# Optimization experiments

Hardware: AMD Instinct MI355X
Metric: run time of the kernel (lower is better)

The kernel has to match this reference:

```python
import jax, jax.numpy as jnp
import numpy as np

DIM = 1024
HEADS = 16
DIM_HEAD = 64
INNER = HEADS * DIM_HEAD
SCALE = DIM_HEAD ** -0.5


def setup_inputs() -> dict:
    key = jax.random.key(0)
    kx, kq, kk, kv, ko = jax.random.split(key, 5)
    B, N = 2, 2048
    s = DIM ** -0.5
    return {
        "x": jax.random.normal(kx, (B, N, DIM), dtype=jnp.float32),
        "Wq": jax.random.normal(kq, (DIM, INNER), dtype=jnp.float32) * s,
        "Wk": jax.random.normal(kk, (DIM, INNER), dtype=jnp.float32) * s,
        "Wv": jax.random.normal(kv, (DIM, INNER), dtype=jnp.float32) * s,
        "Wo": jax.random.normal(ko, (INNER, DIM), dtype=jnp.float32) * s,
    }


def reference(x, Wq, Wk, Wv, Wo):
    B, N, _ = x.shape
    # projections, split heads: b n (h d) -> b h n d
    def split(t):
        return t.reshape(B, N, HEADS, DIM_HEAD).transpose(0, 2, 1, 3)
    q = split(x @ Wq)
    k = split(x @ Wk)
    v = split(x @ Wv)
    # scores [B,H,N,N]
    dots = jnp.einsum("bhnd,bhmd->bhnm", q, k) * SCALE
    # causal mask: positions j > i masked
    causal = jnp.triu(jnp.ones((N, N), dtype=bool), k=1)
    dots = jnp.where(causal, -jnp.inf, dots)
    attn = jax.nn.softmax(dots, axis=-1)
    out = jnp.einsum("bhnm,bhmd->bhnd", attn, v)
    out = out.transpose(0, 2, 1, 3).reshape(B, N, INNER)
    return out @ Wo
```

## Files before the change

kernel.cpp:

```cpp
#include <hip/hip_runtime.h>

typedef unsigned short u16;
typedef unsigned int u32;
typedef __attribute__((ext_vector_type(8))) short short8;
typedef __attribute__((ext_vector_type(4))) short s16x4;
typedef __attribute__((ext_vector_type(4))) float f32x4;
typedef __attribute__((ext_vector_type(16))) float f32x16;
typedef __attribute__((ext_vector_type(4))) u32 u32x4;

typedef const __attribute__((address_space(1))) void* gptr_t;
typedef __attribute__((address_space(3))) void* sptr_t;

#define N_SEQ 2048
#define DIM 1024
#define INNER 1024
#define NTOK 4096
#define QKV_LD 3072

__device__ __forceinline__ u16 f2b(float f) {
  union { float f; unsigned u; } v; v.f = f;
  unsigned r = v.u + 0x7fffu + ((v.u >> 16) & 1u);
  return (u16)(r >> 16);
}

__global__ __launch_bounds__(256) void cast_x_kernel(const float* __restrict__ src,
                                                     u16* __restrict__ dst) {
  const size_t i = (size_t)blockIdx.x * 256 + threadIdx.x;
  const f32x4* s = (const f32x4*)(src + i * 8);
  f32x4 a = s[0], b = s[1];
  short8 o;
#pragma unroll
  for (int j = 0; j < 4; ++j) { o[j] = (short)f2b(a[j]); o[4 + j] = (short)f2b(b[j]); }
  *(short8*)(dst + i * 8) = o;
}

__global__ __launch_bounds__(256) void transpose_cast_kernel(const float* __restrict__ src,
                                                             u16* __restrict__ dst) {
  __shared__ u16 tile[64][65];
  const int n0 = blockIdx.x * 64, k0 = blockIdx.y * 64;
  for (int i = threadIdx.x; i < 4096; i += 256) {
    const int r = i >> 6, c = i & 63;
    tile[r][c] = f2b(src[(size_t)(k0 + r) * 1024 + n0 + c]);
  }
  __syncthreads();
  for (int i = threadIdx.x; i < 4096; i += 256) {
    const int r = i >> 6, c = i & 63;
    dst[(size_t)(n0 + r) * 1024 + k0 + c] = tile[c][r];
  }
}

__global__ __launch_bounds__(256) void transpose_v_kernel(const u16* __restrict__ qkv,
                                                          u16* __restrict__ vt) {
  __shared__ u16 t[64][72];
  const int nt0 = blockIdx.x * 64;
  const int bh = blockIdx.y;
  const int b = bh >> 4, h = bh & 15;
  const u16* src = qkv + (size_t)b * N_SEQ * QKV_LD + 2048 + h * 64;
#pragma unroll
  for (int i = 0; i < 2; ++i) {
    const int cid = i * 256 + threadIdx.x;
    const int r = cid >> 3, c = (cid & 7) * 8;
    *(short8*)&t[r][c] = *(const short8*)(src + (size_t)(nt0 + r) * QKV_LD + c);
  }
  __syncthreads();
#pragma unroll
  for (int i = 0; i < 2; ++i) {
    const int cid = i * 256 + threadIdx.x;
    const int d = cid >> 3, c = (cid & 7) * 8;
    short8 v;
#pragma unroll
    for (int j = 0; j < 8; ++j) v[j] = t[c + j][d];
    *(short8*)(vt + ((size_t)bh * 64 + d) * N_SEQ + nt0 + c) = v;
  }
}

template <typename OutT>
__global__ __launch_bounds__(256) void gemm_tn(const u16* __restrict__ A,
                                               const u16* __restrict__ Bt,
                                               OutT* __restrict__ C,
                                               int M, int N, int K) {
  __shared__ u16 Al[128 * 64];
  __shared__ u16 Bl[128 * 64];
  const int tid = threadIdx.x;
  const int w = tid >> 6, lane = tid & 63;
  const int l15 = lane & 15, lg = lane >> 4;
  const int wr = w >> 1, wc = w & 1;
  const int nwg = gridDim.x * gridDim.y;
  int bid = blockIdx.y * gridDim.x + blockIdx.x;
  bid = (bid & 7) * (nwg >> 3) + (bid >> 3);
  const int bx = bid % gridDim.x, by = bid / gridDim.x;
  const int m0 = by * 128, n0 = bx * 128;

  f32x4 acc[4][4] = {};

  for (int k0 = 0; k0 < K; k0 += 64) {
#pragma unroll
    for (int i = 0; i < 4; ++i) {
      const int chunk = (w << 2) + i;
      const int e = (chunk << 9) + lane * 8;
      const int row = e >> 6, col = e & 63;
      const u16* ga = A + (size_t)(m0 + row) * K + k0 + col;
      __builtin_amdgcn_global_load_lds((gptr_t)ga, (sptr_t)(Al + (chunk << 9)), 16, 0, 0);
      const u16* gb = Bt + (size_t)(n0 + row) * K + k0 + col;
      __builtin_amdgcn_global_load_lds((gptr_t)gb, (sptr_t)(Bl + (chunk << 9)), 16, 0, 0);
    }
    __syncthreads();
#pragma unroll
    for (int kk = 0; kk < 2; ++kk) {
      short8 af[4], bf[4];
#pragma unroll
      for (int m = 0; m < 4; ++m)
        af[m] = *(const short8*)(Al + ((wr * 64 + m * 16 + l15) << 6) + kk * 32 + lg * 8);
#pragma unroll
      for (int n = 0; n < 4; ++n)
        bf[n] = *(const short8*)(Bl + ((wc * 64 + n * 16 + l15) << 6) + kk * 32 + lg * 8);
#pragma unroll
      for (int m = 0; m < 4; ++m)
#pragma unroll
        for (int n = 0; n < 4; ++n)
          acc[m][n] = __builtin_amdgcn_mfma_f32_16x16x32_bf16(af[m], bf[n], acc[m][n], 0, 0, 0);
    }
    __syncthreads();
  }

#pragma unroll
  for (int m = 0; m < 4; ++m)
#pragma unroll
    for (int n = 0; n < 4; ++n)
#pragma unroll
      for (int r = 0; r < 4; ++r) {
        const int row = m0 + wr * 64 + m * 16 + lg * 4 + r;
        const int col = n0 + wc * 64 + n * 16 + l15;
        const float v = acc[m][n][r];
        if constexpr (sizeof(OutT) == 2) C[(size_t)row * N + col] = (OutT)f2b(v);
        else                             C[(size_t)row * N + col] = (OutT)v;
      }
}

__global__ __launch_bounds__(256) void attn_kernel(const u16* __restrict__ qkv,
                                                   const u16* __restrict__ vt,
                                                   u16* __restrict__ attnb) {
  const int bh = blockIdx.x;
  const int qt = 15 - (int)blockIdx.y;
  const int b = bh >> 4, h = bh & 15;
  const int tid = threadIdx.x;
  const int lane = tid & 63, w = tid >> 6;
  const int l31 = lane & 31, hh = lane >> 5;
  const int q0 = qt * 128;
  const int qrow = q0 + w * 32 + l31;

  __shared__ u16 Kl[128 * 64];
  __shared__ u16 Vl[64 * 128];

  const u16* base  = qkv + (size_t)b * N_SEQ * QKV_LD;
  const u16* kbase = base + 1024 + h * 64;
  const u16* vbase = vt + (size_t)bh * 64 * N_SEQ;

  short8 bq[4];
#pragma unroll
  for (int ks = 0; ks < 4; ++ks)
    bq[ks] = *(const short8*)(base + (size_t)qrow * QKV_LD + h * 64 + ks * 16 + hh * 8);

  f32x16 o0 = {}, o1 = {};
  float m_run = -3.0e38f, l_run = 0.f;
  const float kscale = 0.125f * 1.4426950408889634f;
  const int nt = qt + 1;
  const int wbase = tid & ~63;

  for (int jt = 0; jt < nt; ++jt) {
    const int kv0 = jt * 128;
    __syncthreads();
#pragma unroll
    for (int i = 0; i < 4; ++i) {
      const int cid = i * 256 + tid;
      const int krow = cid >> 3, kc = (cid & 7) ^ (krow & 7);
      const u16* ks = kbase + (size_t)(kv0 + krow) * QKV_LD + kc * 8;
      __builtin_amdgcn_global_load_lds((gptr_t)ks, (sptr_t)(Kl + (i * 256 + wbase) * 8), 16, 0, 0);
      const int vrow = cid >> 4, vc = (cid & 15) ^ (vrow & 15);
      const u16* vs = vbase + (size_t)vrow * N_SEQ + kv0 + vc * 8;
      __builtin_amdgcn_global_load_lds((gptr_t)vs, (sptr_t)(Vl + (i * 256 + wbase) * 8), 16, 0, 0);
    }
    __syncthreads();

    const bool last = (jt == nt - 1);
#pragma unroll
    for (int sub = 0; sub < 2; ++sub) {
      if (last && sub == 1 && w < 2) continue;
      const int kv0s = kv0 + sub * 64;

      f32x16 p0 = {}, p1 = {};
#pragma unroll
      for (int ks = 0; ks < 4; ++ks) {
        const int r0 = sub * 64 + l31;
        const int r1 = r0 + 32;
        short8 ak0 = *(const short8*)(Kl + r0 * 64 + (((ks * 2 + hh) ^ (r0 & 7)) * 8));
        short8 ak1 = *(const short8*)(Kl + r1 * 64 + (((ks * 2 + hh) ^ (r1 & 7)) * 8));
        p0 = __builtin_amdgcn_mfma_f32_32x32x16_bf16(ak0, bq[ks], p0, 0, 0, 0);
        p1 = __builtin_amdgcn_mfma_f32_32x32x16_bf16(ak1, bq[ks], p1, 0, 0, 0);
      }

      if (last) {
        const int kvb = kv0s + 4 * hh;
#pragma unroll
        for (int r = 0; r < 16; ++r) {
          const int off = (r & 3) + 8 * (r >> 2);
          if (kvb + off > qrow)      p0[r] = -3.0e38f;
          if (kvb + 32 + off > qrow) p1[r] = -3.0e38f;
        }
      }

      float mt = -3.0e38f;
#pragma unroll
      for (int r = 0; r < 16; ++r) { mt = fmaxf(mt, p0[r]); mt = fmaxf(mt, p1[r]); }
      mt = fmaxf(mt, __shfl_xor(mt, 32, 64));
      const float mn = fmaxf(m_run, mt);
      const float sf = exp2f((m_run - mn) * kscale);
      m_run = mn;
      float ps = 0.f;
#pragma unroll
      for (int r = 0; r < 16; ++r) {
        const float e0 = exp2f((p0[r] - mn) * kscale);
        const float e1 = exp2f((p1[r] - mn) * kscale);
        p0[r] = e0; p1[r] = e1;
        ps += e0 + e1;
      }
      ps += __shfl_xor(ps, 32, 64);
      l_run = l_run * sf + ps;
      o0 *= sf; o1 *= sf;

      u32 bpw[4][4];
#define PACK_TILE(P, kf)                                                    \
      {                                                                     \
        _Pragma("unroll")                                                   \
        for (int a2 = 0; a2 < 2; ++a2) {                                    \
          _Pragma("unroll")                                                 \
          for (int c2 = 0; c2 < 2; ++c2) {                                  \
            u32 X, Y;                                                       \
            asm("v_cvt_pk_bf16_f32 %0, %1, %2" : "=v"(X)                    \
                : "v"(P[8 * a2 + 2 * c2]), "v"(P[8 * a2 + 2 * c2 + 1]));    \
            asm("v_cvt_pk_bf16_f32 %0, %1, %2" : "=v"(Y)                    \
                : "v"(P[8 * a2 + 4 + 2 * c2]), "v"(P[8 * a2 + 5 + 2 * c2]));\
            asm("v_permlane32_swap_b32 %0, %1" : "+v"(X), "+v"(Y));         \
            bpw[(kf) * 2 + a2][c2] = X;                   \
            bpw[(kf) * 2 + a2][2 + c2] = Y;               \
          }                                                                 \
        }                                                                   \
      }
      PACK_TILE(p0, 0)
      PACK_TILE(p1, 1)
#undef PACK_TILE

#pragma unroll
      for (int ks16 = 0; ks16 < 4; ++ks16) {
        u32x4 t = {bpw[ks16][0], bpw[ks16][1], bpw[ks16][2], bpw[ks16][3]};
        short8 bp = __builtin_bit_cast(short8, t);
        const int cb = sub * 8 + ks16 * 2 + hh;
        const int row0 = l31;
        const int row1 = 32 + l31;
        short8 av0 = *(const short8*)(Vl + row0 * 128 + ((cb ^ (row0 & 15)) * 8));
        short8 av1 = *(const short8*)(Vl + row1 * 128 + ((cb ^ (row1 & 15)) * 8));
        o0 = __builtin_amdgcn_mfma_f32_32x32x16_bf16(av0, bp, o0, 0, 0, 0);
        o1 = __builtin_amdgcn_mfma_f32_32x32x16_bf16(av1, bp, o1, 0, 0, 0);
      }
    }
  }

  const float inv = 1.f / l_run;
  u16* orow = attnb + ((size_t)b * N_SEQ + qrow) * INNER + h * 64 + 4 * hh;
#pragma unroll
  for (int rq = 0; rq < 4; ++rq) {
    s16x4 sv0, sv1;
#pragma unroll
    for (int j = 0; j < 4; ++j) {
      sv0[j] = (short)f2b(o0[rq * 4 + j] * inv);
      sv1[j] = (short)f2b(o1[rq * 4 + j] * inv);
    }
    *(s16x4*)(orow + rq * 8) = sv0;
    *(s16x4*)(orow + 32 + rq * 8) = sv1;
  }
}

extern "C" void kernel_launch(void* const* d_in, const int* in_sizes, int n_in,
                              void* d_out, int out_size, void* d_ws, size_t ws_size,
                              hipStream_t stream) {
  const float* x  = (const float*)d_in[0];
  const float* Wq = (const float*)d_in[1];
  const float* Wk = (const float*)d_in[2];
  const float* Wv = (const float*)d_in[3];
  const float* Wo = (const float*)d_in[4];
  float* out = (float*)d_out;

  u16* xb    = (u16*)d_ws;
  u16* wqkvt = xb    + (size_t)NTOK * DIM;
  u16* wot   = wqkvt + (size_t)3 * INNER * DIM;
  u16* qkv   = wot   + (size_t)DIM * INNER;
  u16* attnb = qkv   + (size_t)NTOK * QKV_LD;
  u16* vtb   = attnb + (size_t)NTOK * INNER;

  cast_x_kernel<<<dim3(NTOK * DIM / (256 * 8)), 256, 0, stream>>>(x, xb);
  transpose_cast_kernel<<<dim3(16, 16), 256, 0, stream>>>(Wq, wqkvt);
  transpose_cast_kernel<<<dim3(16, 16), 256, 0, stream>>>(Wk, wqkvt + (size_t)1024 * 1024);
  transpose_cast_kernel<<<dim3(16, 16), 256, 0, stream>>>(Wv, wqkvt + (size_t)2048 * 1024);
  transpose_cast_kernel<<<dim3(16, 16), 256, 0, stream>>>(Wo, wot);

  gemm_tn<u16><<<dim3(3072 / 128, 4096 / 128), 256, 0, stream>>>(xb, wqkvt, qkv, NTOK, 3072, DIM);
  transpose_v_kernel<<<dim3(32, 32), 256, 0, stream>>>(qkv, vtb);
  attn_kernel<<<dim3(32, 16), 256, 0, stream>>>(qkv, vtb, attnb);
  gemm_tn<float><<<dim3(1024 / 128, 4096 / 128), 256, 0, stream>>>(attnb, wot, out, NTOK, INNER, INNER);
}
```

Before: 158.8 us.

## Double-buffer K/V tiles in attention, add lazy softmax rescale and MFMA priority

Switches the attention kernel's K/V shared-memory tiles to double buffering. The next tile is prefetched with global_load_lds while the current tile is computed, so each iteration no longer waits on its load between two barriers. It also skips the running-max rescale of the output accumulators unless the max grows past a threshold, and raises wave priority around the MFMA loops. The cost is doubled LDS use, which may lower occupancy, and hand-written vmcnt waits whose correctness depends on exact load counts.

```diff
diff --git a/kernel.cpp b/kernel.cpp
--- a/kernel.cpp
+++ b/kernel.cpp
@@ -149,8 +149,8 @@
   const int q0 = qt * 128;
   const int qrow = q0 + w * 32 + l31;
 
-  __shared__ u16 Kl[128 * 64];
-  __shared__ u16 Vl[64 * 128];
+  __shared__ u16 Kl[2][128 * 64];
+  __shared__ u16 Vl[2][64 * 128];
 
   const u16* base  = qkv + (size_t)b * N_SEQ * QKV_LD;
   const u16* kbase = base + 1024 + h * 64;
@@ -167,21 +167,40 @@
   const int nt = qt + 1;
   const int wbase = tid & ~63;
 
+#define STAGE(jt_, bufsel)                                                          \
+  {                                                                                 \
+    const int kv0_ = (jt_) * 128;                                                   \
+    u16* Klb = Kl[bufsel];                                                          \
+    u16* Vlb = Vl[bufsel];                                                          \
+    _Pragma("unroll")                                                               \
+    for (int i = 0; i < 4; ++i) {                                                   \
+      const int cid = i * 256 + tid;                                                \
+      const int krow = cid >> 3, kc = (cid & 7) ^ (krow & 7);                       \
+      const u16* ksp = kbase + (size_t)(kv0_ + krow) * QKV_LD + kc * 8;             \
+      __builtin_amdgcn_global_load_lds((gptr_t)ksp,                                 \
+          (sptr_t)(Klb + (i * 256 + wbase) * 8), 16, 0, 0);                         \
+      const int vrow = cid >> 4, vc = (cid & 15) ^ (vrow & 15);                     \
+      const u16* vsp = vbase + (size_t)vrow * N_SEQ + kv0_ + vc * 8;                \
+      __builtin_amdgcn_global_load_lds((gptr_t)vsp,                                 \
+          (sptr_t)(Vlb + (i * 256 + wbase) * 8), 16, 0, 0);                         \
+    }                                                                               \
+  }
+
+  STAGE(0, 0)
+
   for (int jt = 0; jt < nt; ++jt) {
     const int kv0 = jt * 128;
-    __syncthreads();
-#pragma unroll
-    for (int i = 0; i < 4; ++i) {
-      const int cid = i * 256 + tid;
-      const int krow = cid >> 3, kc = (cid & 7) ^ (krow & 7);
-      const u16* ks = kbase + (size_t)(kv0 + krow) * QKV_LD + kc * 8;
-      __builtin_amdgcn_global_load_lds((gptr_t)ks, (sptr_t)(Kl + (i * 256 + wbase) * 8), 16, 0, 0);
-      const int vrow = cid >> 4, vc = (cid & 15) ^ (vrow & 15);
-      const u16* vs = vbase + (size_t)vrow * N_SEQ + kv0 + vc * 8;
-      __builtin_amdgcn_global_load_lds((gptr_t)vs, (sptr_t)(Vl + (i * 256 + wbase) * 8), 16, 0, 0);
-    }
-    __syncthreads();
-
+    const int cur = jt & 1;
+    if (jt + 1 < nt) {
+      STAGE(jt + 1, cur ^ 1)
+      asm volatile("s_waitcnt vmcnt(8)" ::: "memory");
+    } else {
+      asm volatile("s_waitcnt vmcnt(0)" ::: "memory");
+    }
+    __builtin_amdgcn_s_barrier();
+
+    const u16* Klb = Kl[cur];
+    const u16* Vlb = Vl[cur];
     const bool last = (jt == nt - 1);
 #pragma unroll
     for (int sub = 0; sub < 2; ++sub) {
@@ -189,15 +208,17 @@
       const int kv0s = kv0 + sub * 64;
 
       f32x16 p0 = {}, p1 = {};
+      __builtin_amdgcn_s_setprio(1);
 #pragma unroll
       for (int ks = 0; ks < 4; ++ks) {
         const int r0 = sub * 64 + l31;
         const int r1 = r0 + 32;
-        short8 ak0 = *(const short8*)(Kl + r0 * 64 + (((ks * 2 + hh) ^ (r0 & 7)) * 8));
-        short8 ak1 = *(const short8*)(Kl + r1 * 64 + (((ks * 2 + hh) ^ (r1 & 7)) * 8));
+        short8 ak0 = *(const short8*)(Klb + r0 * 64 + (((ks * 2 + hh) ^ (r0 & 7)) * 8));
+        short8 ak1 = *(const short8*)(Klb + r1 * 64 + (((ks * 2 + hh) ^ (r1 & 7)) * 8));
         p0 = __builtin_amdgcn_mfma_f32_32x32x16_bf16(ak0, bq[ks], p0, 0, 0, 0);
         p1 = __builtin_amdgcn_mfma_f32_32x32x16_bf16(ak1, bq[ks], p1, 0, 0, 0);
       }
+      __builtin_amdgcn_s_setprio(0);
 
       if (last) {
         const int kvb = kv0s + 4 * hh;
@@ -214,19 +235,22 @@
       for (int r = 0; r < 16; ++r) { mt = fmaxf(mt, p0[r]); mt = fmaxf(mt, p1[r]); }
       mt = fmaxf(mt, __shfl_xor(mt, 32, 64));
       const float mn = fmaxf(m_run, mt);
-      const float sf = exp2f((m_run - mn) * kscale);
-      m_run = mn;
+      if (!__all(mn - m_run <= 44.f)) {
+        const float sf = exp2f((m_run - mn) * kscale);
+        m_run = mn;
+        l_run *= sf;
+        o0 *= sf; o1 *= sf;
+      }
       float ps = 0.f;
 #pragma unroll
       for (int r = 0; r < 16; ++r) {
-        const float e0 = exp2f((p0[r] - mn) * kscale);
-        const float e1 = exp2f((p1[r] - mn) * kscale);
+        const float e0 = exp2f((p0[r] - m_run) * kscale);
+        const float e1 = exp2f((p1[r] - m_run) * kscale);
         p0[r] = e0; p1[r] = e1;
         ps += e0 + e1;
       }
       ps += __shfl_xor(ps, 32, 64);
-      l_run = l_run * sf + ps;
-      o0 *= sf; o1 *= sf;
+      l_run += ps;
 
       u32 bpw[4][4];
 #define PACK_TILE(P, kf)                                                    \
@@ -241,8 +265,8 @@
             asm("v_cvt_pk_bf16_f32 %0, %1, %2" : "=v"(Y)                    \
                 : "v"(P[8 * a2 + 4 + 2 * c2]), "v"(P[8 * a2 + 5 + 2 * c2]));\
             asm("v_permlane32_swap_b32 %0, %1" : "+v"(X), "+v"(Y));         \
-            bpw[(kf) * 2 + a2][c2] = X;                   \
-            bpw[(kf) * 2 + a2][2 + c2] = Y;               \
+            bpw[(kf) * 2 + a2][c2] = X;                                     \
+            bpw[(kf) * 2 + a2][2 + c2] = Y;                                 \
           }                                                                 \
         }                                                                   \
       }
@@ -250,6 +274,7 @@
       PACK_TILE(p1, 1)
 #undef PACK_TILE
 
+      __builtin_amdgcn_s_setprio(1);
 #pragma unroll
       for (int ks16 = 0; ks16 < 4; ++ks16) {
         u32x4 t = {bpw[ks16][0], bpw[ks16][1], bpw[ks16][2], bpw[ks16][3]};
@@ -257,13 +282,16 @@
         const int cb = sub * 8 + ks16 * 2 + hh;
         const int row0 = l31;
         const int row1 = 32 + l31;
-        short8 av0 = *(const short8*)(Vl + row0 * 128 + ((cb ^ (row0 & 15)) * 8));
-        short8 av1 = *(const short8*)(Vl + row1 * 128 + ((cb ^ (row1 & 15)) * 8));
+        short8 av0 = *(const short8*)(Vlb + row0 * 128 + ((cb ^ (row0 & 15)) * 8));
+        short8 av1 = *(const short8*)(Vlb + row1 * 128 + ((cb ^ (row1 & 15)) * 8));
         o0 = __builtin_amdgcn_mfma_f32_32x32x16_bf16(av0, bp, o0, 0, 0, 0);
         o1 = __builtin_amdgcn_mfma_f32_32x32x16_bf16(av1, bp, o1, 0, 0, 0);
       }
-    }
-  }
+      __builtin_amdgcn_s_setprio(0);
+    }
+    __builtin_amdgcn_s_barrier();
+  }
+#undef STAGE
 
   const float inv = 1.f / l_run;
   u16* orow = attnb + ((size_t)b * N_SEQ + qrow) * INNER + h * 64 + 4 * hh;
```

After: 164.0 us. 1.03x slower.

## Drop LDS staging in attention; per-wave direct K/V loads with lazy rescale

Applied to the files above, without the earlier changes.

Removes the shared-memory K/V tiles and block-wide barriers so each wave independently loads its 64-key K and V fragments straight from global memory into registers. Each wave now runs over only its own causal range, using 64-key steps. It also adds lazy softmax rescaling, which skips the exp and accumulator rescale unless the max rises past a threshold, and adds s_setprio around the MFMA bursts. The trade is that waves in a block no longer share K/V loads, so global/L2 traffic rises and latency may be exposed without a software pipeline.

```diff
diff --git a/kernel.cpp b/kernel.cpp
--- a/kernel.cpp
+++ b/kernel.cpp
@@ -141,16 +141,13 @@
                                                    const u16* __restrict__ vt,
                                                    u16* __restrict__ attnb) {
   const int bh = blockIdx.x;
-  const int qt = 15 - (int)blockIdx.y;
   const int b = bh >> 4, h = bh & 15;
   const int tid = threadIdx.x;
   const int lane = tid & 63, w = tid >> 6;
   const int l31 = lane & 31, hh = lane >> 5;
-  const int q0 = qt * 128;
-  const int qrow = q0 + w * 32 + l31;
-
-  __shared__ u16 Kl[128 * 64];
-  __shared__ u16 Vl[64 * 128];
+  const int qw = (15 - (int)blockIdx.y) * 4 + w;
+  const int q0 = qw * 32;
+  const int qrow = q0 + l31;
 
   const u16* base  = qkv + (size_t)b * N_SEQ * QKV_LD;
   const u16* kbase = base + 1024 + h * 64;
@@ -164,105 +161,100 @@
   f32x16 o0 = {}, o1 = {};
   float m_run = -3.0e38f, l_run = 0.f;
   const float kscale = 0.125f * 1.4426950408889634f;
-  const int nt = qt + 1;
-  const int wbase = tid & ~63;
+  const int nt = (qw >> 1) + 1;
 
   for (int jt = 0; jt < nt; ++jt) {
-    const int kv0 = jt * 128;
-    __syncthreads();
-#pragma unroll
-    for (int i = 0; i < 4; ++i) {
-      const int cid = i * 256 + tid;
-      const int krow = cid >> 3, kc = (cid & 7) ^ (krow & 7);
-      const u16* ks = kbase + (size_t)(kv0 + krow) * QKV_LD + kc * 8;
-      __builtin_amdgcn_global_load_lds((gptr_t)ks, (sptr_t)(Kl + (i * 256 + wbase) * 8), 16, 0, 0);
-      const int vrow = cid >> 4, vc = (cid & 15) ^ (vrow & 15);
-      const u16* vs = vbase + (size_t)vrow * N_SEQ + kv0 + vc * 8;
-      __builtin_amdgcn_global_load_lds((gptr_t)vs, (sptr_t)(Vl + (i * 256 + wbase) * 8), 16, 0, 0);
-    }
-    __syncthreads();
-
-    const bool last = (jt == nt - 1);
-#pragma unroll
-    for (int sub = 0; sub < 2; ++sub) {
-      if (last && sub == 1 && w < 2) continue;
-      const int kv0s = kv0 + sub * 64;
-
-      f32x16 p0 = {}, p1 = {};
-#pragma unroll
-      for (int ks = 0; ks < 4; ++ks) {
-        const int r0 = sub * 64 + l31;
-        const int r1 = r0 + 32;
-        short8 ak0 = *(const short8*)(Kl + r0 * 64 + (((ks * 2 + hh) ^ (r0 & 7)) * 8));
-        short8 ak1 = *(const short8*)(Kl + r1 * 64 + (((ks * 2 + hh) ^ (r1 & 7)) * 8));
-        p0 = __builtin_amdgcn_mfma_f32_32x32x16_bf16(ak0, bq[ks], p0, 0, 0, 0);
-        p1 = __builtin_amdgcn_mfma_f32_32x32x16_bf16(ak1, bq[ks], p1, 0, 0, 0);
+    const int kvs = jt * 64;
+
+    const u16* kr0 = kbase + (size_t)(kvs + l31) * QKV_LD + hh * 8;
+    const u16* kr1 = kbase + (size_t)(kvs + 32 + l31) * QKV_LD + hh * 8;
+    short8 ak0[4], ak1[4];
+#pragma unroll
+    for (int ks = 0; ks < 4; ++ks) {
+      ak0[ks] = *(const short8*)(kr0 + ks * 16);
+      ak1[ks] = *(const short8*)(kr1 + ks * 16);
+    }
+    const u16* vr0 = vbase + (size_t)l31 * N_SEQ + kvs + hh * 8;
+    const u16* vr1 = vbase + (size_t)(32 + l31) * N_SEQ + kvs + hh * 8;
+    short8 av0[4], av1[4];
+#pragma unroll
+    for (int ks = 0; ks < 4; ++ks) {
+      av0[ks] = *(const short8*)(vr0 + ks * 16);
+      av1[ks] = *(const short8*)(vr1 + ks * 16);
+    }
+
+    f32x16 p0 = {}, p1 = {};
+    __builtin_amdgcn_s_setprio(1);
+#pragma unroll
+    for (int ks = 0; ks < 4; ++ks) {
+      p0 = __builtin_amdgcn_mfma_f32_32x32x16_bf16(ak0[ks], bq[ks], p0, 0, 0, 0);
+      p1 = __builtin_amdgcn_mfma_f32_32x32x16_bf16(ak1[ks], bq[ks], p1, 0, 0, 0);
+    }
+    __builtin_amdgcn_s_setprio(0);
+
+    if (jt == nt - 1) {
+      const int kvb = kvs + 4 * hh;
+#pragma unroll
+      for (int r = 0; r < 16; ++r) {
+        const int off = (r & 3) + 8 * (r >> 2);
+        if (kvb + off > qrow)      p0[r] = -3.0e38f;
+        if (kvb + 32 + off > qrow) p1[r] = -3.0e38f;
       }
-
-      if (last) {
-        const int kvb = kv0s + 4 * hh;
-#pragma unroll
-        for (int r = 0; r < 16; ++r) {
-          const int off = (r & 3) + 8 * (r >> 2);
-          if (kvb + off > qrow)      p0[r] = -3.0e38f;
-          if (kvb + 32 + off > qrow) p1[r] = -3.0e38f;
-        }
-      }
-
-      float mt = -3.0e38f;
-#pragma unroll
-      for (int r = 0; r < 16; ++r) { mt = fmaxf(mt, p0[r]); mt = fmaxf(mt, p1[r]); }
-      mt = fmaxf(mt, __shfl_xor(mt, 32, 64));
-      const float mn = fmaxf(m_run, mt);
+    }
+
+    float mt = -3.0e38f;
+#pragma unroll
+    for (int r = 0; r < 16; ++r) { mt = fmaxf(mt, p0[r]); mt = fmaxf(mt, p1[r]); }
+    mt = fmaxf(mt, __shfl_xor(mt, 32, 64));
+    const float mn = fmaxf(m_run, mt);
+    if (!__all(mn - m_run <= 44.f)) {
       const float sf = exp2f((m_run - mn) * kscale);
       m_run = mn;
-      float ps = 0.f;
-#pragma unroll
-      for (int r = 0; r < 16; ++r) {
-        const float e0 = exp2f((p0[r] - mn) * kscale);
-        const float e1 = exp2f((p1[r] - mn) * kscale);
-        p0[r] = e0; p1[r] = e1;
-        ps += e0 + e1;
-      }
-      ps += __shfl_xor(ps, 32, 64);
-      l_run = l_run * sf + ps;
+      l_run *= sf;
       o0 *= sf; o1 *= sf;
-
-      u32 bpw[4][4];
+    }
+    float ps = 0.f;
+#pragma unroll
+    for (int r = 0; r < 16; ++r) {
+      const float e0 = exp2f((p0[r] - m_run) * kscale);
+      const float e1 = exp2f((p1[r] - m_run) * kscale);
+      p0[r] = e0; p1[r] = e1;
+      ps += e0 + e1;
+    }
+    ps += __shfl_xor(ps, 32, 64);
+    l_run += ps;
+
+    u32 bpw[4][4];
 #define PACK_TILE(P, kf)                                                    \
-      {                                                                     \
+    {                                                                       \
+      _Pragma("unroll")                                                     \
+      for (int a2 = 0; a2 < 2; ++a2) {                                      \
         _Pragma("unroll")                                                   \
-        for (int a2 = 0; a2 < 2; ++a2) {                                    \
-          _Pragma("unroll")                                                 \
-          for (int c2 = 0; c2 < 2; ++c2) {                                  \
-            u32 X, Y;                                                       \
-            asm("v_cvt_pk_bf16_f32 %0, %1, %2" : "=v"(X)                    \
-                : "v"(P[8 * a2 + 2 * c2]), "v"(P[8 * a2 + 2 * c2 + 1]));    \
-            asm("v_cvt_pk_bf16_f32 %0, %1, %2" : "=v"(Y)                    \
-                : "v"(P[8 * a2 + 4 + 2 * c2]), "v"(P[8 * a2 + 5 + 2 * c2]));\
-            asm("v_permlane32_swap_b32 %0, %1" : "+v"(X), "+v"(Y));         \
-            bpw[(kf) * 2 + a2][c2] = X;                   \
-            bpw[(kf) * 2 + a2][2 + c2] = Y;               \
-          }                                                                 \
+        for (int c2 = 0; c2 < 2; ++c2) {                                    \
+          u32 X, Y;                                                         \
+          asm("v_cvt_pk_bf16_f32 %0, %1, %2" : "=v"(X)                      \
+              : "v"(P[8 * a2 + 2 * c2]), "v"(P[8 * a2 + 2 * c2 + 1]));      \
+          asm("v_cvt_pk_bf16_f32 %0, %1, %2" : "=v"(Y)                      \
+              : "v"(P[8 * a2 + 4 + 2 * c2]), "v"(P[8 * a2 + 5 + 2 * c2]));  \
+          asm("v_permlane32_swap_b32 %0, %1" : "+v"(X), "+v"(Y));           \
+          bpw[(kf) * 2 + a2][c2] = X;                                       \
+          bpw[(kf) * 2 + a2][2 + c2] = Y;                                   \
         }                                                                   \
-      }
-      PACK_TILE(p0, 0)
-      PACK_TILE(p1, 1)
+      }                                                                     \
+    }
+    PACK_TILE(p0, 0)
+    PACK_TILE(p1, 1)
 #undef PACK_TILE
 
-#pragma unroll
-      for (int ks16 = 0; ks16 < 4; ++ks16) {
-        u32x4 t = {bpw[ks16][0], bpw[ks16][1], bpw[ks16][2], bpw[ks16][3]};
-        short8 bp = __builtin_bit_cast(short8, t);
-        const int cb = sub * 8 + ks16 * 2 + hh;
-        const int row0 = l31;
-        const int row1 = 32 + l31;
-        short8 av0 = *(const short8*)(Vl + row0 * 128 + ((cb ^ (row0 & 15)) * 8));
-        short8 av1 = *(const short8*)(Vl + row1 * 128 + ((cb ^ (row1 & 15)) * 8));
-        o0 = __builtin_amdgcn_mfma_f32_32x32x16_bf16(av0, bp, o0, 0, 0, 0);
-        o1 = __builtin_amdgcn_mfma_f32_32x32x16_bf16(av1, bp, o1, 0, 0, 0);
-      }
-    }
+    __builtin_amdgcn_s_setprio(1);
+#pragma unroll
+    for (int ks16 = 0; ks16 < 4; ++ks16) {
+      u32x4 t = {bpw[ks16][0], bpw[ks16][1], bpw[ks16][2], bpw[ks16][3]};
+      short8 bp = __builtin_bit_cast(short8, t);
+      o0 = __builtin_amdgcn_mfma_f32_32x32x16_bf16(av0[ks16], bp, o0, 0, 0, 0);
+      o1 = __builtin_amdgcn_mfma_f32_32x32x16_bf16(av1[ks16], bp, o1, 0, 0, 0);
+    }
+    __builtin_amdgcn_s_setprio(0);
   }
 
   const float inv = 1.f / l_run;
```

Measured after the change: 193.1 us. +21.6%, slower.
